# Performance work log

Measured on AMD Instinct MI355X. Metric: run time of the kernel, lower is better.

Reference implementation:

```python
import jax, jax.numpy as jnp
import numpy as np

D_MODEL = 1024
NUM_HEADS = 16
D_H = D_MODEL // NUM_HEADS
BATCH, SEQ = 4, 2048


def setup_inputs() -> dict:
    key = jax.random.key(0)
    kx, kq, kk, kv, ko = jax.random.split(key, 5)
    sigma = (2.0 / (D_MODEL + D_MODEL)) ** 0.5

    def trunc(k):
        return jax.random.truncated_normal(k, -3.0, 3.0, (D_MODEL, D_MODEL), dtype=jnp.float32) * sigma

    return {
        "x": jax.random.normal(kx, (BATCH, SEQ, D_MODEL), dtype=jnp.float32),
        "Wq": trunc(kq),
        "Wk": trunc(kk),
        "Wv": trunc(kv),
        "Wo": trunc(ko),
    }


def reference(x, Wq, Wk, Wv, Wo):
    B, S, D = x.shape
    H, Dh = NUM_HEADS, D_H
    # Linear: einsum('d_out d_in, ... d_in -> ... d_out')
    q = jnp.einsum('oi,bsi->bso', Wq, x)
    k = jnp.einsum('oi,bsi->bso', Wk, x)
    v = jnp.einsum('oi,bsi->bso', Wv, x)
    # split heads: [B, H, S, Dh]
    q = q.reshape(B, S, H, Dh).transpose(0, 2, 1, 3)
    k = k.reshape(B, S, H, Dh).transpose(0, 2, 1, 3)
    v = v.reshape(B, S, H, Dh).transpose(0, 2, 1, 3)
    scale = 1.0 / jnp.sqrt(jnp.asarray(Dh, dtype=x.dtype))
    score = jnp.einsum('bhnd,bhmd->bhnm', q, k) * scale  # [B,H,S,S]
    causal = jnp.tril(jnp.ones((S, S), dtype=bool))
    score = jnp.where(causal, score, -jnp.inf)
    attn = jax.nn.softmax(score, axis=-1)
    out = jnp.einsum('bhnm,bhmd->bhnd', attn, v)
    out = out.transpose(0, 2, 1, 3).reshape(B, S, D)
    return jnp.einsum('oi,bsi->bso', Wo, out)
```

## Files before the change

kernel.cpp:

```cpp
#include <hip/hip_runtime.h>
#include <hip/hip_bf16.h>

typedef __bf16 bf16x8 __attribute__((ext_vector_type(8)));
typedef __bf16 bf16x4 __attribute__((ext_vector_type(4)));
typedef float f32x4 __attribute__((ext_vector_type(4)));
typedef float f32x16 __attribute__((ext_vector_type(16)));

#define NB 4
#define NS 2048
#define ND 1024
#define NH 16
#define NDH 64
#define NM (NB*NS)

#define MFMA(a,b,c)   __builtin_amdgcn_mfma_f32_16x16x32_bf16((a),(b),(c),0,0,0)
#define MFMA32(a,b,c) __builtin_amdgcn_mfma_f32_32x32x16_bf16((a),(b),(c),0,0,0)

__device__ __forceinline__ void gload16(const void* g, void* l) {
    __builtin_amdgcn_global_load_lds(
        (const __attribute__((address_space(1))) void*)(g),
        (__attribute__((address_space(3))) void*)(l),
        16, 0, 0);
}

__device__ __forceinline__ unsigned cvt_pk_bf16(float lo, float hi) {
    unsigned w;
    asm("v_cvt_pk_bf16_f32 %0, %1, %2" : "=v"(w) : "v"(lo), "v"(hi));
    return w;
}
#define PLSWAP(a, b) asm("v_permlane32_swap_b32 %0, %1" : "+v"(a), "+v"(b))

__global__ __launch_bounds__(256) void cast4(const float* __restrict__ in,
                                             __bf16* __restrict__ out, int n) {
    int i = (blockIdx.x * 256 + threadIdx.x) * 4;
    if (i >= n) return;
    float4 v = *(const float4*)(in + i);
    bf16x4 o;
    o[0] = (__bf16)v.x; o[1] = (__bf16)v.y; o[2] = (__bf16)v.z; o[3] = (__bf16)v.w;
    *(bf16x4*)(out + i) = o;
}

template<int MODE>
__global__ __launch_bounds__(256) void gemm128(
    const __bf16* __restrict__ A,
    const __bf16* __restrict__ W0, const __bf16* __restrict__ W1,
    const __bf16* __restrict__ W2,
    __bf16* __restrict__ O0, __bf16* __restrict__ O1, __bf16* __restrict__ O2,
    float* __restrict__ Cf)
{
    __shared__ alignas(16) __bf16 As[128*32];
    __shared__ alignas(16) __bf16 Bs[128*32];

    const int tid  = threadIdx.x;
    const int wave = tid >> 6, lane = tid & 63;
    const int l16  = lane & 15, lq = lane >> 4;
    const int bm = blockIdx.x * 128;
    const int bn = blockIdx.y * 128;
    const int z  = (MODE == 0) ? blockIdx.z : 0;
    const __bf16* __restrict__ Bw =
        (MODE == 0) ? ((z == 0) ? W0 : (z == 1) ? W1 : W2) : W0;

    const int wr = (wave >> 1) * 64;
    const int wc = (wave & 1) * 64;

    f32x4 acc[4][4];
    #pragma unroll
    for (int i = 0; i < 4; i++)
        #pragma unroll
        for (int j = 0; j < 4; j++)
            acc[i][j] = (f32x4){0.f, 0.f, 0.f, 0.f};

    const int ch0 = tid, ch1 = tid + 256;
    const int r0 = ch0 >> 2, c0 = (ch0 & 3) * 8;
    const int r1 = ch1 >> 2, c1 = (ch1 & 3) * 8;

    for (int k0 = 0; k0 < ND; k0 += 32) {
        __syncthreads();
        gload16(A  + (size_t)(bm + r0) * ND + k0 + c0, As + ch0 * 8);
        gload16(Bw + (size_t)(bn + r0) * ND + k0 + c0, Bs + ch0 * 8);
        gload16(A  + (size_t)(bm + r1) * ND + k0 + c1, As + ch1 * 8);
        gload16(Bw + (size_t)(bn + r1) * ND + k0 + c1, Bs + ch1 * 8);
        __syncthreads();

        bf16x8 af[4], bf[4];
        #pragma unroll
        for (int i = 0; i < 4; i++) {
            af[i] = *(const bf16x8*)(As + (wr + i*16 + l16) * 32 + lq * 8);
            bf[i] = *(const bf16x8*)(Bs + (wc + i*16 + l16) * 32 + lq * 8);
        }
        #pragma unroll
        for (int i = 0; i < 4; i++)
            #pragma unroll
            for (int j = 0; j < 4; j++)
                acc[i][j] = MFMA(af[i], bf[j], acc[i][j]);
    }

    #pragma unroll
    for (int i = 0; i < 4; i++) {
        #pragma unroll
        for (int j = 0; j < 4; j++) {
            #pragma unroll
            for (int r = 0; r < 4; r++) {
                int row = bm + wr + i*16 + lq*4 + r;
                int col = bn + wc + j*16 + l16;
                float v = acc[i][j][r];
                if (MODE == 1) {
                    Cf[(size_t)row * ND + col] = v;
                } else {
                    if (z == 0) v *= 0.1803368801111204f;
                    int b = row >> 11, s = row & 2047;
                    int h = col >> 6,  dh = col & 63;
                    if (z < 2) {
                        __bf16* dst = (z == 0) ? O0 : O1;
                        dst[(((size_t)b*NH + h)*NS + s)*NDH + dh] = (__bf16)v;
                    } else {
                        O2[(((size_t)b*NH + h)*NDH + dh)*NS + s] = (__bf16)v;
                    }
                }
            }
        }
    }
}

__global__ __launch_bounds__(256) void attn_st(
    const __bf16* __restrict__ Q, const __bf16* __restrict__ K,
    const __bf16* __restrict__ Vt, __bf16* __restrict__ Oa)
{
    __shared__ alignas(16) __bf16 Ks[32*64];
    __shared__ alignas(16) __bf16 Vs[64*32];
    __shared__ float Fs[4][32];

    const int tid  = threadIdx.x;
    const int wave = tid >> 6, lane = tid & 63;
    const int qq   = lane & 31, hi = lane >> 5;

    const int bid = blockIdx.x;
    const int jg  = 15 - (bid >> 6);
    const int bh  = (bid & 7) * 8 + ((bid >> 3) & 7);
    const int j   = 4 * jg + wave;
    const int q0  = 32 * j;
    const int nt  = 4 * jg + 4;

    const int b = bh >> 4, h = bh & 15;
    const size_t qkb = (size_t)bh * NS * NDH;
    const size_t vbb = (size_t)bh * NDH * NS;
    float* Fw = Fs[wave];

    bf16x8 qf[4];
    {
        const __bf16* qr = Q + qkb + (size_t)(q0 + qq) * NDH + hi * 8;
        #pragma unroll
        for (int c = 0; c < 4; c++) qf[c] = *(const bf16x8*)(qr + c * 16);
    }

    f32x16 o0 = (f32x16)0.f, o1 = (f32x16)0.f;
    float mr = -__builtin_inff(), lsum = 0.f;

    const int kr = tid >> 3, ku = tid & 7;
    const int vd = tid >> 2, vu = tid & 3;
    const __bf16* ksrc = K  + qkb + (size_t)kr * NDH + (size_t)((ku ^ (kr & 7)) * 8);
    const __bf16* vsrc = Vt + vbb + (size_t)vd * NS  + (size_t)((vu ^ (vd & 3)) * 8);
    __bf16* kdst = Ks + tid * 8;
    __bf16* vdst = Vs + tid * 8;

    #pragma unroll 1
    for (int t = 0; t < nt; ++t) {
        __syncthreads();
        gload16(ksrc, kdst);
        gload16(vsrc, vdst);
        asm volatile("s_waitcnt vmcnt(0)" ::: "memory");
        __syncthreads();

        if (t <= j) {
            bf16x8 kf[4], vf[4];
            #pragma unroll
            for (int c = 0; c < 4; c++)
                kf[c] = *(const bf16x8*)(Ks + qq * 64 + ((2 * c + hi) ^ (qq & 7)) * 8);
            vf[0] = *(const bf16x8*)(Vs + qq * 32        + ((hi)     ^ (qq & 3)) * 8);
            vf[1] = *(const bf16x8*)(Vs + qq * 32        + ((2 + hi) ^ (qq & 3)) * 8);
            vf[2] = *(const bf16x8*)(Vs + (qq + 32) * 32 + ((hi)     ^ (qq & 3)) * 8);
            vf[3] = *(const bf16x8*)(Vs + (qq + 32) * 32 + ((2 + hi) ^ (qq & 3)) * 8);

            f32x16 s = (f32x16)0.f;
            __builtin_amdgcn_s_setprio(1);
            #pragma unroll
            for (int c = 0; c < 4; c++) s = MFMA32(kf[c], qf[c], s);
            __builtin_amdgcn_s_setprio(0);

            if (t == j) {
                #pragma unroll
                for (int r = 0; r < 16; r++) {
                    const int crow = (r & 3) + 8 * (r >> 2) + 4 * hi;
                    if (crow > qq) s[r] = -__builtin_inff();
                }
            }

            float tm = s[0];
            #pragma unroll
            for (int r = 1; r < 16; r++) tm = fmaxf(tm, s[r]);

            if (__any(tm > mr + 8.f)) {
                float rowm = fmaxf(tm, __shfl_xor(tm, 32));
                float mnew = fmaxf(mr, rowm);
                float fac  = exp2f(mr - mnew);
                mr = mnew; lsum *= fac;
                if (lane < 32) Fw[qq] = fac;
                f32x4 f0 = *(const f32x4*)&Fw[4 * hi];
                f32x4 f1 = *(const f32x4*)&Fw[8 + 4 * hi];
                f32x4 f2 = *(const f32x4*)&Fw[16 + 4 * hi];
                f32x4 f3 = *(const f32x4*)&Fw[24 + 4 * hi];
                #pragma unroll
                for (int i = 0; i < 4; i++) {
                    o0[i]      *= f0[i]; o1[i]      *= f0[i];
                    o0[4 + i]  *= f1[i]; o1[4 + i]  *= f1[i];
                    o0[8 + i]  *= f2[i]; o1[8 + i]  *= f2[i];
                    o0[12 + i] *= f3[i]; o1[12 + i] *= f3[i];
                }
            }

            float pv[16]; float psum = 0.f;
            #pragma unroll
            for (int r = 0; r < 16; r++) { pv[r] = exp2f(s[r] - mr); psum += pv[r]; }
            lsum += psum;

            unsigned w0 = cvt_pk_bf16(pv[0],  pv[1]);
            unsigned w1 = cvt_pk_bf16(pv[2],  pv[3]);
            unsigned w2 = cvt_pk_bf16(pv[4],  pv[5]);
            unsigned w3 = cvt_pk_bf16(pv[6],  pv[7]);
            unsigned w4 = cvt_pk_bf16(pv[8],  pv[9]);
            unsigned w5 = cvt_pk_bf16(pv[10], pv[11]);
            unsigned w6 = cvt_pk_bf16(pv[12], pv[13]);
            unsigned w7 = cvt_pk_bf16(pv[14], pv[15]);
            PLSWAP(w0, w2); PLSWAP(w1, w3);
            PLSWAP(w4, w6); PLSWAP(w5, w7);
            bf16x8 pa0 = __builtin_bit_cast(bf16x8, (uint4){w0, w1, w2, w3});
            bf16x8 pa1 = __builtin_bit_cast(bf16x8, (uint4){w4, w5, w6, w7});

            __builtin_amdgcn_s_setprio(1);
            o0 = MFMA32(pa0, vf[0], o0);
            o0 = MFMA32(pa1, vf[1], o0);
            o1 = MFMA32(pa0, vf[2], o1);
            o1 = MFMA32(pa1, vf[3], o1);
            __builtin_amdgcn_s_setprio(0);
        }

        ksrc += 32 * NDH;
        vsrc += 32;
    }

    lsum += __shfl_xor(lsum, 32);
    if (lane < 32) Fw[qq] = 1.f / lsum;
    f32x4 i0 = *(const f32x4*)&Fw[4 * hi];
    f32x4 i1 = *(const f32x4*)&Fw[8 + 4 * hi];
    f32x4 i2 = *(const f32x4*)&Fw[16 + 4 * hi];
    f32x4 i3 = *(const f32x4*)&Fw[24 + 4 * hi];
    __bf16* ob = Oa + ((size_t)b * NS + q0) * ND + h * 64 + qq;
    #pragma unroll
    for (int g2 = 0; g2 < 4; g2++) {
        f32x4 iv = (g2 == 0) ? i0 : (g2 == 1) ? i1 : (g2 == 2) ? i2 : i3;
        #pragma unroll
        for (int i = 0; i < 4; i++) {
            const int row = 8 * g2 + 4 * hi + i;
            ob[(size_t)row * ND]      = (__bf16)(o0[4 * g2 + i] * iv[i]);
            ob[(size_t)row * ND + 32] = (__bf16)(o1[4 * g2 + i] * iv[i]);
        }
    }
}

extern "C" void kernel_launch(void* const* d_in, const int* in_sizes, int n_in,
                              void* d_out, int out_size, void* d_ws, size_t ws_size,
                              hipStream_t stream) {
    const float* x  = (const float*)d_in[0];
    const float* wq = (const float*)d_in[1];
    const float* wk = (const float*)d_in[2];
    const float* wv = (const float*)d_in[3];
    const float* wo = (const float*)d_in[4];
    char* ws = (char*)d_ws;

    __bf16* xb  = (__bf16*)(ws);
    __bf16* wqb = (__bf16*)(ws + (16ull << 20));
    __bf16* wkb = (__bf16*)(ws + (18ull << 20));
    __bf16* wvb = (__bf16*)(ws + (20ull << 20));
    __bf16* wob = (__bf16*)(ws + (22ull << 20));
    __bf16* Qb  = (__bf16*)(ws + (24ull << 20));
    __bf16* Kb  = (__bf16*)(ws + (40ull << 20));
    __bf16* Vtb = (__bf16*)(ws + (56ull << 20));
    __bf16* Ab  = (__bf16*)(ws + (72ull << 20));
    float* out  = (float*)d_out;

    cast4<<<dim3(NM * ND / 1024), 256, 0, stream>>>(x,  xb,  NM * ND);
    cast4<<<dim3(ND * ND / 1024), 256, 0, stream>>>(wq, wqb, ND * ND);
    cast4<<<dim3(ND * ND / 1024), 256, 0, stream>>>(wk, wkb, ND * ND);
    cast4<<<dim3(ND * ND / 1024), 256, 0, stream>>>(wv, wvb, ND * ND);
    cast4<<<dim3(ND * ND / 1024), 256, 0, stream>>>(wo, wob, ND * ND);

    gemm128<0><<<dim3(NM/128, ND/128, 3), 256, 0, stream>>>(
        xb, wqb, wkb, wvb, Qb, Kb, Vtb, nullptr);

    attn_st<<<dim3(1024), 256, 0, stream>>>(Qb, Kb, Vtb, Ab);

    gemm128<1><<<dim3(NM/128, ND/128), 256, 0, stream>>>(
        Ab, wob, nullptr, nullptr, nullptr, nullptr, nullptr, out);
}
```

Measured before the change: 207.7 us.

## Stage V-transpose through LDS, fuse weight casts, retune V swizzle, use max3

The V projection output is now transposed through shared memory and written as 16-byte vectors along the sequence dimension, replacing scattered 2-byte strided stores. The four weight-cast launches are merged into one launch with a grid y dimension of 4, saving launch overhead. The LDS XOR swizzle for the V tile is changed to index on (row>>1) to reduce bank conflicts, and the row-max reduction uses v_max3_f32. Costs are extra LDS syncs in the V-epilogue, and the swizzle change must stay consistent between the global-load and LDS-read sides.

```diff
diff --git a/kernel.cpp b/kernel.cpp
--- a/kernel.cpp
+++ b/kernel.cpp
@@ -27,6 +27,11 @@
     unsigned w;
     asm("v_cvt_pk_bf16_f32 %0, %1, %2" : "=v"(w) : "v"(lo), "v"(hi));
     return w;
+}
+__device__ __forceinline__ float fmax3(float a, float b, float c) {
+    float d;
+    asm("v_max3_f32 %0, %1, %2, %3" : "=v"(d) : "v"(a), "v"(b), "v"(c));
+    return d;
 }
 #define PLSWAP(a, b) asm("v_permlane32_swap_b32 %0, %1" : "+v"(a), "+v"(b))
 
@@ -40,6 +45,21 @@
     *(bf16x4*)(out + i) = o;
 }
 
+__global__ __launch_bounds__(256) void cast4w(
+    const float* __restrict__ w0, const float* __restrict__ w1,
+    const float* __restrict__ w2, const float* __restrict__ w3,
+    __bf16* __restrict__ o0, __bf16* __restrict__ o1,
+    __bf16* __restrict__ o2, __bf16* __restrict__ o3) {
+    const int z = blockIdx.y;
+    const float* in  = (z == 0) ? w0 : (z == 1) ? w1 : (z == 2) ? w2 : w3;
+    __bf16*      out = (z == 0) ? o0 : (z == 1) ? o1 : (z == 2) ? o2 : o3;
+    int i = (blockIdx.x * 256 + threadIdx.x) * 4;
+    float4 v = *(const float4*)(in + i);
+    bf16x4 o;
+    o[0] = (__bf16)v.x; o[1] = (__bf16)v.y; o[2] = (__bf16)v.z; o[3] = (__bf16)v.w;
+    *(bf16x4*)(out + i) = o;
+}
+
 template<int MODE>
 __global__ __launch_bounds__(256) void gemm128(
     const __bf16* __restrict__ A,
@@ -48,8 +68,9 @@
     __bf16* __restrict__ O0, __bf16* __restrict__ O1, __bf16* __restrict__ O2,
     float* __restrict__ Cf)
 {
-    __shared__ alignas(16) __bf16 As[128*32];
-    __shared__ alignas(16) __bf16 Bs[128*32];
+    __shared__ alignas(16) __bf16 SB[2 * 128 * 32];
+    __bf16* As = SB;
+    __bf16* Bs = SB + 128 * 32;
 
     const int tid  = threadIdx.x;
     const int wave = tid >> 6, lane = tid & 63;
@@ -93,6 +114,40 @@
             #pragma unroll
             for (int j = 0; j < 4; j++)
                 acc[i][j] = MFMA(af[i], bf[j], acc[i][j]);
+    }
+
+    if (MODE == 0 && z == 2) {
+        __bf16* T = SB;
+        const int TP = 136;
+        #pragma unroll 1
+        for (int c = 0; c < 4; ++c) {
+            __syncthreads();
+            #pragma unroll
+            for (int j = 0; j < 4; j++) {
+                if (((wc + j * 16) >> 5) != c) continue;
+                #pragma unroll
+                for (int i = 0; i < 4; i++)
+                    #pragma unroll
+                    for (int r = 0; r < 4; r++) {
+                        int row = wr + i*16 + lq*4 + r;
+                        int col = wc + j*16 + l16 - c*32;
+                        T[col * TP + row] = (__bf16)acc[i][j][r];
+                    }
+            }
+            __syncthreads();
+            #pragma unroll
+            for (int u2 = 0; u2 < 2; u2++) {
+                int idx  = tid + u2 * 256;
+                int trow = idx >> 4, tu = idx & 15;
+                int gcol = bn + c*32 + trow;
+                int gs   = bm + tu * 8;
+                bf16x8 val = *(const bf16x8*)&T[trow * TP + tu * 8];
+                int hh = gcol >> 6, dh = gcol & 63;
+                *(bf16x8*)&O2[(((size_t)(gs >> 11) * NH + hh) * NDH + dh) * NS
+                              + (gs & 2047)] = val;
+            }
+        }
+        return;
     }
 
     #pragma unroll
@@ -110,12 +165,8 @@
                     if (z == 0) v *= 0.1803368801111204f;
                     int b = row >> 11, s = row & 2047;
                     int h = col >> 6,  dh = col & 63;
-                    if (z < 2) {
-                        __bf16* dst = (z == 0) ? O0 : O1;
-                        dst[(((size_t)b*NH + h)*NS + s)*NDH + dh] = (__bf16)v;
-                    } else {
-                        O2[(((size_t)b*NH + h)*NDH + dh)*NS + s] = (__bf16)v;
-                    }
+                    __bf16* dst = (z == 0) ? O0 : O1;
+                    dst[(((size_t)b*NH + h)*NS + s)*NDH + dh] = (__bf16)v;
                 }
             }
         }
@@ -159,9 +210,11 @@
     const int kr = tid >> 3, ku = tid & 7;
     const int vd = tid >> 2, vu = tid & 3;
     const __bf16* ksrc = K  + qkb + (size_t)kr * NDH + (size_t)((ku ^ (kr & 7)) * 8);
-    const __bf16* vsrc = Vt + vbb + (size_t)vd * NS  + (size_t)((vu ^ (vd & 3)) * 8);
+    const __bf16* vsrc = Vt + vbb + (size_t)vd * NS  + (size_t)((vu ^ ((vd >> 1) & 3)) * 8);
     __bf16* kdst = Ks + tid * 8;
     __bf16* vdst = Vs + tid * 8;
+
+    const int vsw = (qq >> 1) & 3;
 
     #pragma unroll 1
     for (int t = 0; t < nt; ++t) {
@@ -176,10 +229,10 @@
             #pragma unroll
             for (int c = 0; c < 4; c++)
                 kf[c] = *(const bf16x8*)(Ks + qq * 64 + ((2 * c + hi) ^ (qq & 7)) * 8);
-            vf[0] = *(const bf16x8*)(Vs + qq * 32        + ((hi)     ^ (qq & 3)) * 8);
-            vf[1] = *(const bf16x8*)(Vs + qq * 32        + ((2 + hi) ^ (qq & 3)) * 8);
-            vf[2] = *(const bf16x8*)(Vs + (qq + 32) * 32 + ((hi)     ^ (qq & 3)) * 8);
-            vf[3] = *(const bf16x8*)(Vs + (qq + 32) * 32 + ((2 + hi) ^ (qq & 3)) * 8);
+            vf[0] = *(const bf16x8*)(Vs + qq * 32        + ((hi)     ^ vsw) * 8);
+            vf[1] = *(const bf16x8*)(Vs + qq * 32        + ((2 + hi) ^ vsw) * 8);
+            vf[2] = *(const bf16x8*)(Vs + (qq + 32) * 32 + ((hi)     ^ vsw) * 8);
+            vf[3] = *(const bf16x8*)(Vs + (qq + 32) * 32 + ((2 + hi) ^ vsw) * 8);
 
             f32x16 s = (f32x16)0.f;
             __builtin_amdgcn_s_setprio(1);
@@ -195,9 +248,12 @@
                 }
             }
 
-            float tm = s[0];
-            #pragma unroll
-            for (int r = 1; r < 16; r++) tm = fmaxf(tm, s[r]);
+            float a0 = fmax3(s[0],  s[1],  s[2]);
+            float a1 = fmax3(s[3],  s[4],  s[5]);
+            float a2 = fmax3(s[6],  s[7],  s[8]);
+            float a3 = fmax3(s[9],  s[10], s[11]);
+            float a4 = fmax3(s[12], s[13], s[14]);
+            float tm = fmaxf(fmax3(a0, a1, a2), fmax3(a3, a4, s[15]));
 
             if (__any(tm > mr + 8.f)) {
                 float rowm = fmaxf(tm, __shfl_xor(tm, 32));
@@ -288,11 +344,9 @@
     __bf16* Ab  = (__bf16*)(ws + (72ull << 20));
     float* out  = (float*)d_out;
 
-    cast4<<<dim3(NM * ND / 1024), 256, 0, stream>>>(x,  xb,  NM * ND);
-    cast4<<<dim3(ND * ND / 1024), 256, 0, stream>>>(wq, wqb, ND * ND);
-    cast4<<<dim3(ND * ND / 1024), 256, 0, stream>>>(wk, wkb, ND * ND);
-    cast4<<<dim3(ND * ND / 1024), 256, 0, stream>>>(wv, wvb, ND * ND);
-    cast4<<<dim3(ND * ND / 1024), 256, 0, stream>>>(wo, wob, ND * ND);
+    cast4<<<dim3(NM * ND / 1024), 256, 0, stream>>>(x, xb, NM * ND);
+    cast4w<<<dim3(ND * ND / 1024, 4), 256, 0, stream>>>(
+        wq, wk, wv, wo, wqb, wkb, wvb, wob);
 
     gemm128<0><<<dim3(NM/128, ND/128, 3), 256, 0, stream>>>(
         xb, wqb, wkb, wvb, Qb, Kb, Vtb, nullptr);
```

New measurement: 186.9 us. 1.11x faster.
